# Performance work log

Measured on AMD Instinct MI355X. Metric: run time of the kernel, lower is better.

Reference implementation:

```python
import jax, jax.numpy as jnp
import numpy as np

V, E, H, OUT, L = 32000, 512, 512, 2, 2
S, B = 512, 64


def setup_inputs() -> dict:
    key = jax.random.key(0)
    ks = jax.random.split(key, 8)
    sc_w = float(np.sqrt(6.0 / (H + (E + H))))  # xavier_uniform bound-ish scale
    inp = {
        "texts": jax.random.randint(ks[0], (S, B), 0, V, dtype=jnp.int64),
        "emb": jax.random.normal(ks[1], (V, E), jnp.float32) * 0.05,
        "Wf": jax.random.normal(ks[2], (L, H, E + H), jnp.float32) * sc_w,
        "bf": jnp.zeros((L, H, 1), jnp.float32),
        "Wi": jax.random.normal(ks[3], (L, H, E + H), jnp.float32) * sc_w,
        "bi": jnp.zeros((L, H, 1), jnp.float32),
        "Wo": jax.random.normal(ks[4], (L, H, E + H), jnp.float32) * sc_w,
        "bo": jnp.zeros((L, H, 1), jnp.float32),
        "Wc": jax.random.normal(ks[5], (L, H, E + H), jnp.float32) * sc_w,
        "bc": jnp.zeros((L, H, 1), jnp.float32),
        "Wy": jax.random.normal(ks[6], (OUT, H), jnp.float32) * 0.05,
        "by": jnp.zeros((OUT, 1), jnp.float32),
    }
    return inp


def reference(texts, emb, Wf, bf, Wi, bi, Wo, bo, Wc, bc, Wy, by):
    seq_len, batch = texts.shape
    num_layers, hidden = Wf.shape[0], Wf.shape[1]
    # embedded: [S, E, B] (matches torch permute(1,2,0) of [B,S,E])
    x_seq = jnp.transpose(emb[texts], (0, 2, 1))

    h0 = jnp.zeros((hidden, batch), x_seq.dtype)
    c0 = jnp.zeros((hidden, batch), x_seq.dtype)

    def step(carry, x):
        h, c = carry  # NOTE: single (h, c) shared across layers, as in source
        for l in range(num_layers):
            cat = jnp.concatenate([h, x], axis=0)  # [H+E, B]
            ft = jax.nn.sigmoid(Wf[l] @ cat + bf[l])
            it = jax.nn.sigmoid(Wi[l] @ cat + bi[l])
            chat = jnp.tanh(Wc[l] @ cat + bc[l])
            c = ft * c + it * chat
            ot = jax.nn.sigmoid(Wo[l] @ cat + bo[l])
            h = ot * jnp.tanh(c)
            x = h
        return (h, c), None

    (h, _), _ = jax.lax.scan(step, (h0, c0), x_seq)
    y = h.T @ Wy.T + by.T  # [B, OUT]
    return jnp.squeeze(y, axis=1) if y.shape[1] == 1 else y
```

## Files before the change

kernel.cpp:

```cpp
#include <hip/hip_runtime.h>


typedef _Float16 f16;
typedef _Float16 f16x8 __attribute__((ext_vector_type(8)));
typedef float f32x4 __attribute__((ext_vector_type(4)));
typedef unsigned int u32;
typedef unsigned long long u64;
typedef unsigned short u16;

constexpr int Hn = 512, En = 512, Bn = 64, Sn = 512, OUTn = 2;
constexpr int NG = 4, GB = 32, BS = 16, RPB = 16;
constexpr int NB = NG * GB;
constexpr int NT = 512;

constexpr size_t XB_OFF = 0;
constexpr size_t XB_SZ  = (size_t)NG * Sn * 16 * 64 * 16;
constexpr size_t HB_OFF = XB_OFF + XB_SZ;
constexpr size_t HB_SZ  = (size_t)NG * 2 * 16384;
constexpr size_t FLAG_OFF = HB_OFF + HB_SZ;
constexpr size_t FLAG_SZ  = (size_t)NG * 4096;

__device__ __forceinline__ float sig_(float x) { return 1.f / (1.f + expf(-x)); }

__device__ __forceinline__ u32 aload(const u32* p) {
  return __hip_atomic_load(p, __ATOMIC_RELAXED, __HIP_MEMORY_SCOPE_AGENT);
}
__device__ __forceinline__ void astore(u32* p, u32 v) {
  __hip_atomic_store(p, v, __ATOMIC_RELAXED, __HIP_MEMORY_SCOPE_AGENT);
}
__device__ __forceinline__ u64 aload64(const u64* p) {
  return __hip_atomic_load(p, __ATOMIC_RELAXED, __HIP_MEMORY_SCOPE_AGENT);
}

union uf16 { f16 f; u16 u; };

__device__ __forceinline__ f16x8 ldfrag2(const u64* base, int frag) {
  union { f16x8 v; u64 q[2]; } u;
  u.q[0] = aload64(base + frag * 2);
  u.q[1] = aload64(base + frag * 2 + 1);
  return u.v;
}

__device__ __forceinline__ int fl_idx(int k, int col) {
  return (((k >> 5) * 64 + (((k >> 3) & 3) * 16) + col) << 3) + (k & 7);
}

__global__ void __launch_bounds__(256) xb_fill(
    const int* __restrict__ texts, const float* __restrict__ emb,
    f16x8* __restrict__ xb)
{
  const int bidx = blockIdx.x;
  const int g = bidx >> 9, t = bidx & (Sn - 1);
  const int tid = threadIdx.x;
  f16x8* dst = xb + (size_t)bidx * 1024;
  for (int slot = tid; slot < 1024; slot += 256) {
    int s = slot >> 6, sl = slot & 63, kg = sl >> 4, b = sl & 15;
    int idx = texts[t * Bn + g * BS + b];
    const float* er = emb + (size_t)idx * En + s * 32 + kg * 8;
    f16x8 v;
    #pragma unroll
    for (int j = 0; j < 8; ++j) v[j] = (f16)er[j];
    dst[slot] = v;
  }
}

__global__ void __launch_bounds__(NT) lstm_mfma(
    const int* __restrict__ texts, const float* __restrict__ emb,
    const float* __restrict__ Wf, const float* __restrict__ bf,
    const float* __restrict__ Wi, const float* __restrict__ bi,
    const float* __restrict__ Wo, const float* __restrict__ bo,
    const float* __restrict__ Wc, const float* __restrict__ bc,
    const float* __restrict__ Wy, const float* __restrict__ by,
    float* __restrict__ out, const f16x8* __restrict__ xb,
    char* __restrict__ hbBase, u32* __restrict__ flagBase)
{
  __shared__ f16x8 sWA0[4][32][64];
  __shared__ f16x8 sHB[1024];
  __shared__ float sAccP[2][64][17];
  __shared__ float sAccX[64][17];
  __shared__ float sBiasX[64], sBias1[64];
  __shared__ float sC[16][16];
  __shared__ f16   sH[16][16];
  __shared__ float sRed[16][2][4];

  const int tid = threadIdx.x;
  const int bid = blockIdx.x;
  const int g = bid & 3;
  const int rank = bid >> 2;
  const int w = tid >> 6, l = tid & 63;
  const int mt = w & 3, kh = w >> 2;
  const int col = l & 15, rb = (l >> 4) << 2;

  const float* Wg[4] = {Wf, Wi, Wc, Wo};
  const float* Bg[4] = {bf, bi, bc, bo};

  u32* hb0 = (u32*)(hbBase + (size_t)(g * 2 + 0) * 16384);
  u32* hb1 = (u32*)(hbBase + (size_t)(g * 2 + 1) * 16384);
  u32* flagG  = flagBase + (size_t)g * 1024;
  u32* myFlag = flagG + rank;
  const f16x8* xbG = xb + (size_t)g * Sn * 1024;

  for (int i = 0; i < 16; ++i) {
    int slot = tid * 16 + i;
    int sl = slot & 63, s = (slot >> 6) & 31, m4 = slot >> 11;
    const float* row = Wg[m4] + (size_t)(rank * RPB + (sl & 15)) * (En + Hn);
    int k0 = s * 32 + (sl >> 4) * 8;
    f16x8 v;
    #pragma unroll
    for (int j = 0; j < 8; ++j) v[j] = (f16)row[k0 + j];
    sWA0[m4][s][sl] = v;
  }
  f16x8 afr1[8];
  {
    const float* row = Wg[mt] + (size_t)(Hn + rank * RPB + (l & 15)) * (En + Hn);
    #pragma unroll
    for (int i = 0; i < 8; ++i) {
      int k0 = (kh * 8 + i) * 32 + (l >> 4) * 8;
      f16x8 v;
      #pragma unroll
      for (int j = 0; j < 8; ++j) v[j] = (f16)(row[k0 + j] + row[k0 + j + Hn]);
      afr1[i] = v;
    }
  }
  if (tid < 64) {
    int gate = tid >> 4, hr = tid & 15;
    sBiasX[tid] = Bg[gate][rank * RPB + hr];
    sBias1[tid] = Bg[gate][Hn + rank * RPB + hr];
  }
  if (tid < 256) sC[tid >> 4][tid & 15] = 0.f;
  for (int i = tid; i < 4096; i += NT) astore(hb0 + i, 0u);
  __syncthreads();

  if (kh == 1) {
    f32x4 acc = {0.f, 0.f, 0.f, 0.f};
    #pragma unroll
    for (int s = 0; s < 16; ++s)
      acc = __builtin_amdgcn_mfma_f32_16x16x32_f16(sWA0[mt][16 + s][l], xbG[s * 64 + l], acc, 0, 0, 0);
    #pragma unroll
    for (int v = 0; v < 4; ++v) sAccX[mt * 16 + rb + v][col] = acc[v];
  }

  u32 phase = 0;

  __syncthreads();
  ++phase;
  if (tid == 0) astore(myFlag, phase);
  if (tid < 32) {
    u32 v = aload(flagG + tid);
    while (__any(v < phase)) { __builtin_amdgcn_s_sleep(1); v = aload(flagG + tid); }
  }
  __syncthreads();

  for (int t = 0; t < Sn; ++t) {
    {
      const u64* src = (const u64*)hb0;
      #pragma unroll
      for (int j = 0; j < 2; ++j) { int f = w * 128 + j * 64 + l; sHB[f] = ldfrag2(src, f); }
    }
    __syncthreads();
    {
      f32x4 acc = {0.f, 0.f, 0.f, 0.f};
      #pragma unroll
      for (int i = 0; i < 8; ++i) {
        int s = kh * 8 + i;
        acc = __builtin_amdgcn_mfma_f32_16x16x32_f16(sWA0[mt][s][l], sHB[s * 64 + l], acc, 0, 0, 0);
      }
      #pragma unroll
      for (int v = 0; v < 4; ++v) sAccP[kh][mt * 16 + rb + v][col] = acc[v];
    }
    __syncthreads();
    if (tid < 256) {
      int hr = tid >> 4, b = tid & 15;
      float af = sAccP[0][ 0 + hr][b] + sAccP[1][ 0 + hr][b] + sAccX[ 0 + hr][b] + sBiasX[ 0 + hr];
      float ai = sAccP[0][16 + hr][b] + sAccP[1][16 + hr][b] + sAccX[16 + hr][b] + sBiasX[16 + hr];
      float ac = sAccP[0][32 + hr][b] + sAccP[1][32 + hr][b] + sAccX[32 + hr][b] + sBiasX[32 + hr];
      float ao = sAccP[0][48 + hr][b] + sAccP[1][48 + hr][b] + sAccX[48 + hr][b] + sBiasX[48 + hr];
      float ft = sig_(af), it = sig_(ai), ch = tanhf(ac), ot = sig_(ao);
      float c = ft * sC[hr][b] + it * ch;
      sC[hr][b] = c;
      sH[hr][b] = (f16)(ot * tanhf(c));
    }
    __syncthreads();
    if (tid < 128) {
      int q = tid >> 4, b = tid & 15;
      int k0 = rank * RPB + 2 * q;
      uf16 lo, hi; lo.f = sH[2 * q][b]; hi.f = sH[2 * q + 1][b];
      int slot = (k0 >> 5) * 64 + ((k0 >> 3) & 3) * 16 + b;
      astore(hb1 + slot * 4 + (q & 3), (u32)lo.u | ((u32)hi.u << 16));
    }
    __syncthreads();
    ++phase;
    if (tid == 0) astore(myFlag, phase);
    if (tid < 32) {
      u32 v = aload(flagG + tid);
      while (__any(v < phase)) { __builtin_amdgcn_s_sleep(1); v = aload(flagG + tid); }
    }
    __syncthreads();

    {
      const u64* src = (const u64*)hb1;
      #pragma unroll
      for (int j = 0; j < 2; ++j) { int f = w * 128 + j * 64 + l; sHB[f] = ldfrag2(src, f); }
    }
    __syncthreads();
    {
      f32x4 acc = {0.f, 0.f, 0.f, 0.f};
      #pragma unroll
      for (int i = 0; i < 8; ++i)
        acc = __builtin_amdgcn_mfma_f32_16x16x32_f16(afr1[i], sHB[(kh * 8 + i) * 64 + l], acc, 0, 0, 0);
      #pragma unroll
      for (int v = 0; v < 4; ++v) sAccP[kh][mt * 16 + rb + v][col] = acc[v];
    }
    __syncthreads();
    if (tid < 256) {
      int hr = tid >> 4, b = tid & 15;
      float af = sAccP[0][ 0 + hr][b] + sAccP[1][ 0 + hr][b] + sBias1[ 0 + hr];
      float ai = sAccP[0][16 + hr][b] + sAccP[1][16 + hr][b] + sBias1[16 + hr];
      float ac = sAccP[0][32 + hr][b] + sAccP[1][32 + hr][b] + sBias1[32 + hr];
      float ao = sAccP[0][48 + hr][b] + sAccP[1][48 + hr][b] + sBias1[48 + hr];
      float ft = sig_(af), it = sig_(ai), ch = tanhf(ac), ot = sig_(ao);
      float c = ft * sC[hr][b] + it * ch;
      sC[hr][b] = c;
      sH[hr][b] = (f16)(ot * tanhf(c));
    }
    __syncthreads();
    if (tid < 128) {
      int q = tid >> 4, b = tid & 15;
      int k0 = rank * RPB + 2 * q;
      uf16 lo, hi; lo.f = sH[2 * q][b]; hi.f = sH[2 * q + 1][b];
      int slot = (k0 >> 5) * 64 + ((k0 >> 3) & 3) * 16 + b;
      astore(hb0 + slot * 4 + (q & 3), (u32)lo.u | ((u32)hi.u << 16));
    }
    __syncthreads();
    ++phase;
    if (tid == 0) astore(myFlag, phase);
    if (kh == 1 && t + 1 < Sn) {
      const f16x8* xbt = xbG + (size_t)(t + 1) * 1024;
      f32x4 acc = {0.f, 0.f, 0.f, 0.f};
      #pragma unroll
      for (int s = 0; s < 16; ++s)
        acc = __builtin_amdgcn_mfma_f32_16x16x32_f16(sWA0[mt][16 + s][l], xbt[s * 64 + l], acc, 0, 0, 0);
      #pragma unroll
      for (int v = 0; v < 4; ++v) sAccX[mt * 16 + rb + v][col] = acc[v];
    }
    if (tid < 32) {
      u32 v = aload(flagG + tid);
      while (__any(v < phase)) { __builtin_amdgcn_s_sleep(1); v = aload(flagG + tid); }
    }
    __syncthreads();
  }

  if (rank == 0) {
    f16* tmp = (f16*)&sWA0[0][0][0];
    for (int i = tid; i < 4096; i += NT) ((u32*)tmp)[i] = aload(hb0 + i);
    __syncthreads();
    if (tid < 128) {
      int b = tid >> 3, o = (tid >> 2) & 1, kc = tid & 3;
      float p = 0.f;
      for (int kk = 0; kk < 128; ++kk) {
        int k = kc * 128 + kk;
        p += (float)tmp[fl_idx(k, b)] * Wy[o * Hn + k];
      }
      sRed[b][o][kc] = p;
    }
    __syncthreads();
    if (tid < 32) {
      int b2 = tid >> 1, o2 = tid & 1;
      float s = by[o2];
      #pragma unroll
      for (int q = 0; q < 4; ++q) s += sRed[b2][o2][q];
      out[(g * BS + b2) * OUTn + o2] = s;
    }
  }
}

extern "C" void kernel_launch(void* const* d_in, const int* in_sizes, int n_in,
                              void* d_out, int out_size, void* d_ws, size_t ws_size,
                              hipStream_t stream) {
  const int*   texts = (const int*)d_in[0];
  const float* emb   = (const float*)d_in[1];
  const float* Wf    = (const float*)d_in[2];
  const float* bf    = (const float*)d_in[3];
  const float* Wi    = (const float*)d_in[4];
  const float* bi    = (const float*)d_in[5];
  const float* Wo    = (const float*)d_in[6];
  const float* bo    = (const float*)d_in[7];
  const float* Wc    = (const float*)d_in[8];
  const float* bc    = (const float*)d_in[9];
  const float* Wy    = (const float*)d_in[10];
  const float* by    = (const float*)d_in[11];
  float* out = (float*)d_out;

  f16x8* xbuf     = (f16x8*)((char*)d_ws + XB_OFF);
  char*  hbBase   = (char*)d_ws + HB_OFF;
  u32*   flagBase = (u32*)((char*)d_ws + FLAG_OFF);
  hipMemsetAsync((void*)flagBase, 0, FLAG_SZ, stream);

  xb_fill<<<dim3(NG * Sn), dim3(256), 0, stream>>>(texts, emb, xbuf);

  void* args[] = {(void*)&texts, (void*)&emb, (void*)&Wf, (void*)&bf, (void*)&Wi, (void*)&bi,
                  (void*)&Wo, (void*)&bo, (void*)&Wc, (void*)&bc, (void*)&Wy, (void*)&by,
                  (void*)&out, (void*)&xbuf, (void*)&hbBase, (void*)&flagBase};
  hipLaunchCooperativeKernel((const void*)lstm_mfma, dim3(NB), dim3(NT), args, 0, stream);
}
```

Baseline: 2.712 ms.

## Move x-weights to registers, prefetch x into LDS, shrink barrier and flag handshake

New measurement: 2.797 ms. 1.03x slower.

```diff
diff --git a/kernel.cpp b/kernel.cpp
--- a/kernel.cpp
+++ b/kernel.cpp
@@ -74,7 +74,8 @@
     float* __restrict__ out, const f16x8* __restrict__ xb,
     char* __restrict__ hbBase, u32* __restrict__ flagBase)
 {
-  __shared__ f16x8 sWA0[4][32][64];
+  __shared__ f16x8 sWAh[4][16][64];
+  __shared__ f16x8 sXB[16][64];
   __shared__ f16x8 sHB[1024];
   __shared__ float sAccP[2][64][17];
   __shared__ float sAccX[64][17];
@@ -100,15 +101,15 @@
   u32* myFlag = flagG + rank;
   const f16x8* xbG = xb + (size_t)g * Sn * 1024;
 
-  for (int i = 0; i < 16; ++i) {
-    int slot = tid * 16 + i;
-    int sl = slot & 63, s = (slot >> 6) & 31, m4 = slot >> 11;
+  for (int i = 0; i < 8; ++i) {
+    int slot = tid * 8 + i;
+    int sl = slot & 63, s = (slot >> 6) & 15, m4 = slot >> 10;
     const float* row = Wg[m4] + (size_t)(rank * RPB + (sl & 15)) * (En + Hn);
     int k0 = s * 32 + (sl >> 4) * 8;
     f16x8 v;
     #pragma unroll
     for (int j = 0; j < 8; ++j) v[j] = (f16)row[k0 + j];
-    sWA0[m4][s][sl] = v;
+    sWAh[m4][s][sl] = v;
   }
   f16x8 afr1[8];
   {
@@ -120,6 +121,18 @@
       #pragma unroll
       for (int j = 0; j < 8; ++j) v[j] = (f16)(row[k0 + j] + row[k0 + j + Hn]);
       afr1[i] = v;
+    }
+  }
+  f16x8 axf[16];
+  if (kh == 1) {
+    const float* row = Wg[mt] + (size_t)(rank * RPB + (l & 15)) * (En + Hn);
+    #pragma unroll
+    for (int i = 0; i < 16; ++i) {
+      int k0 = Hn + i * 32 + (l >> 4) * 8;
+      f16x8 v;
+      #pragma unroll
+      for (int j = 0; j < 8; ++j) v[j] = (f16)row[k0 + j];
+      axf[i] = v;
     }
   }
   if (tid < 64) {
@@ -131,31 +144,40 @@
   for (int i = tid; i < 4096; i += NT) astore(hb0 + i, 0u);
   __syncthreads();
 
+  {
+    f16x8 a = xbG[w * 128 + l], b = xbG[w * 128 + 64 + l];
+    sXB[2 * w][l] = a; sXB[2 * w + 1][l] = b;
+  }
+  __syncthreads();
   if (kh == 1) {
     f32x4 acc = {0.f, 0.f, 0.f, 0.f};
     #pragma unroll
     for (int s = 0; s < 16; ++s)
-      acc = __builtin_amdgcn_mfma_f32_16x16x32_f16(sWA0[mt][16 + s][l], xbG[s * 64 + l], acc, 0, 0, 0);
+      acc = __builtin_amdgcn_mfma_f32_16x16x32_f16(axf[s], sXB[s][l], acc, 0, 0, 0);
     #pragma unroll
     for (int v = 0; v < 4; ++v) sAccX[mt * 16 + rb + v][col] = acc[v];
   }
-
-  u32 phase = 0;
-
   __syncthreads();
-  ++phase;
-  if (tid == 0) astore(myFlag, phase);
-  if (tid < 32) {
-    u32 v = aload(flagG + tid);
-    while (__any(v < phase)) { __builtin_amdgcn_s_sleep(1); v = aload(flagG + tid); }
+
+  u32 phase = 1;
+  if (w == 0) {
+    asm volatile("s_waitcnt vmcnt(0)" ::: "memory");
+    if (l == 0) astore(myFlag, phase);
+    u32 v = aload(flagG + (l & 31));
+    while (__any(v < phase)) { __builtin_amdgcn_s_sleep(1); v = aload(flagG + (l & 31)); }
   }
   __syncthreads();
 
   for (int t = 0; t < Sn; ++t) {
+    const int tn = (t + 1 < Sn) ? t + 1 : t;
+    const f16x8* xbt = xbG + (size_t)tn * 1024;
+    f16x8 xp0 = xbt[w * 128 + l];
+    f16x8 xp1 = xbt[w * 128 + 64 + l];
     {
       const u64* src = (const u64*)hb0;
-      #pragma unroll
-      for (int j = 0; j < 2; ++j) { int f = w * 128 + j * 64 + l; sHB[f] = ldfrag2(src, f); }
+      f16x8 a = ldfrag2(src, w * 128 + l);
+      f16x8 b = ldfrag2(src, w * 128 + 64 + l);
+      sHB[w * 128 + l] = a; sHB[w * 128 + 64 + l] = b;
     }
     __syncthreads();
     {
@@ -163,7 +185,7 @@
       #pragma unroll
       for (int i = 0; i < 8; ++i) {
         int s = kh * 8 + i;
-        acc = __builtin_amdgcn_mfma_f32_16x16x32_f16(sWA0[mt][s][l], sHB[s * 64 + l], acc, 0, 0, 0);
+        acc = __builtin_amdgcn_mfma_f32_16x16x32_f16(sWAh[mt][s][l], sHB[s * 64 + l], acc, 0, 0, 0);
       }
       #pragma unroll
       for (int v = 0; v < 4; ++v) sAccP[kh][mt * 16 + rb + v][col] = acc[v];
@@ -181,26 +203,31 @@
       sH[hr][b] = (f16)(ot * tanhf(c));
     }
     __syncthreads();
-    if (tid < 128) {
-      int q = tid >> 4, b = tid & 15;
-      int k0 = rank * RPB + 2 * q;
-      uf16 lo, hi; lo.f = sH[2 * q][b]; hi.f = sH[2 * q + 1][b];
-      int slot = (k0 >> 5) * 64 + ((k0 >> 3) & 3) * 16 + b;
-      astore(hb1 + slot * 4 + (q & 3), (u32)lo.u | ((u32)hi.u << 16));
-    }
-    __syncthreads();
     ++phase;
-    if (tid == 0) astore(myFlag, phase);
-    if (tid < 32) {
-      u32 v = aload(flagG + tid);
-      while (__any(v < phase)) { __builtin_amdgcn_s_sleep(1); v = aload(flagG + tid); }
+    if (w == 0) {
+      #pragma unroll
+      for (int j = 0; j < 2; ++j) {
+        int idx = j * 64 + l, q = idx >> 4, b_ = idx & 15;
+        int k0 = rank * RPB + 2 * q;
+        uf16 lo, hi; lo.f = sH[2 * q][b_]; hi.f = sH[2 * q + 1][b_];
+        int slot = (k0 >> 5) * 64 + ((k0 >> 3) & 3) * 16 + b_;
+        astore(hb1 + slot * 4 + (q & 3), (u32)lo.u | ((u32)hi.u << 16));
+      }
+      asm volatile("s_waitcnt vmcnt(0)" ::: "memory");
+      if (l == 0) astore(myFlag, phase);
+    }
+    sXB[2 * w][l] = xp0; sXB[2 * w + 1][l] = xp1;
+    if (w == 0) {
+      u32 v = aload(flagG + (l & 31));
+      while (__any(v < phase)) { __builtin_amdgcn_s_sleep(1); v = aload(flagG + (l & 31)); }
     }
     __syncthreads();
 
     {
       const u64* src = (const u64*)hb1;
-      #pragma unroll
-      for (int j = 0; j < 2; ++j) { int f = w * 128 + j * 64 + l; sHB[f] = ldfrag2(src, f); }
+      f16x8 a = ldfrag2(src, w * 128 + l);
+      f16x8 b = ldfrag2(src, w * 128 + 64 + l);
+      sHB[w * 128 + l] = a; sHB[w * 128 + 64 + l] = b;
     }
     __syncthreads();
     {
@@ -224,36 +251,39 @@
       sH[hr][b] = (f16)(ot * tanhf(c));
     }
     __syncthreads();
-    if (tid < 128) {
-      int q = tid >> 4, b = tid & 15;
-      int k0 = rank * RPB + 2 * q;
-      uf16 lo, hi; lo.f = sH[2 * q][b]; hi.f = sH[2 * q + 1][b];
-      int slot = (k0 >> 5) * 64 + ((k0 >> 3) & 3) * 16 + b;
-      astore(hb0 + slot * 4 + (q & 3), (u32)lo.u | ((u32)hi.u << 16));
-    }
-    __syncthreads();
     ++phase;
-    if (tid == 0) astore(myFlag, phase);
+    if (w == 0) {
+      #pragma unroll
+      for (int j = 0; j < 2; ++j) {
+        int idx = j * 64 + l, q = idx >> 4, b_ = idx & 15;
+        int k0 = rank * RPB + 2 * q;
+        uf16 lo, hi; lo.f = sH[2 * q][b_]; hi.f = sH[2 * q + 1][b_];
+        int slot = (k0 >> 5) * 64 + ((k0 >> 3) & 3) * 16 + b_;
+        astore(hb0 + slot * 4 + (q & 3), (u32)lo.u | ((u32)hi.u << 16));
+      }
+      asm volatile("s_waitcnt vmcnt(0)" ::: "memory");
+      if (l == 0) astore(myFlag, phase);
+    }
     if (kh == 1 && t + 1 < Sn) {
-      const f16x8* xbt = xbG + (size_t)(t + 1) * 1024;
       f32x4 acc = {0.f, 0.f, 0.f, 0.f};
       #pragma unroll
       for (int s = 0; s < 16; ++s)
-        acc = __builtin_amdgcn_mfma_f32_16x16x32_f16(sWA0[mt][16 + s][l], xbt[s * 64 + l], acc, 0, 0, 0);
+        acc = __builtin_amdgcn_mfma_f32_16x16x32_f16(axf[s], sXB[s][l], acc, 0, 0, 0);
       #pragma unroll
       for (int v = 0; v < 4; ++v) sAccX[mt * 16 + rb + v][col] = acc[v];
     }
-    if (tid < 32) {
-      u32 v = aload(flagG + tid);
-      while (__any(v < phase)) { __builtin_amdgcn_s_sleep(1); v = aload(flagG + tid); }
+    if (w == 0) {
+      u32 v = aload(flagG + (l & 31));
+      while (__any(v < phase)) { __builtin_amdgcn_s_sleep(1); v = aload(flagG + (l & 31)); }
     }
     __syncthreads();
   }
 
   if (rank == 0) {
-    f16* tmp = (f16*)&sWA0[0][0][0];
-    for (int i = tid; i < 4096; i += NT) ((u32*)tmp)[i] = aload(hb0 + i);
-    __syncthreads();
+    u32* tmpu = (u32*)sHB;
+    for (int i = tid; i < 4096; i += NT) tmpu[i] = aload(hb0 + i);
+    __syncthreads();
+    const f16* tmp = (const f16*)sHB;
     if (tid < 128) {
       int b = tid >> 3, o = (tid >> 2) & 1, kc = tid & 3;
       float p = 0.f;
```
